# Kernel tuning notes

Measured on AMD Instinct MI355X. Metric: run time of the kernel, lower is better.

Reference implementation:

```python
import jax, jax.numpy as jnp
import numpy as np

B, L, DIM = 16, 1024, 768
HEADS, DIM_HEAD = 12, 64
INNER = HEADS * DIM_HEAD  # 768


def _make_perm(key, l, dim):
    # first `dim` entries identity, rest a random permutation of [dim, l*dim)
    tail = dim + jax.random.permutation(key, (l - 1) * dim)
    return jnp.concatenate([jnp.arange(dim), tail]).astype(jnp.int32)


def setup_inputs() -> dict:
    key = jax.random.key(0)
    kx, kq, kk, kv, ko, kp1, kp2 = jax.random.split(key, 7)
    s = DIM ** -0.5
    return {
        "x": jax.random.normal(kx, (B, L, DIM), dtype=jnp.float32),
        "Wq": jax.random.normal(kq, (DIM, INNER), dtype=jnp.float32) * s,
        "Wk": jax.random.normal(kk, (DIM, INNER), dtype=jnp.float32) * s,
        "Wv": jax.random.normal(kv, (DIM, INNER), dtype=jnp.float32) * s,
        "Wo": jax.random.normal(ko, (INNER, DIM), dtype=jnp.float32) * (INNER ** -0.5),
        "bo": jnp.zeros((DIM,), dtype=jnp.float32),
        "permq": _make_perm(kp1, L, DIM),
        "permk": _make_perm(kp2, L, DIM),
    }


def reference(x, Wq, Wk, Wv, Wo, bo, permq, permk):
    b, l, d = x.shape
    scale = DIM_HEAD ** -0.5
    flat = x.reshape(b, l * d)
    xq = flat[:, permq].reshape(b, l, d)  # irregular gather across (seq*dim)
    xk = flat[:, permk].reshape(b, l, d)
    # projections + head split: b n (h d) -> b h n d
    q = (xq @ Wq).reshape(b, l, HEADS, DIM_HEAD).transpose(0, 2, 1, 3)
    k = (xk @ Wk).reshape(b, l, HEADS, DIM_HEAD).transpose(0, 2, 1, 3)
    v = (x @ Wv).reshape(b, l, HEADS, DIM_HEAD).transpose(0, 2, 1, 3)
    dots = jnp.einsum('bhnd,bhmd->bhnm', q, k) * scale
    attn = jax.nn.softmax(dots, axis=-1)
    out = jnp.einsum('bhnm,bhmd->bhnd', attn, v)
    out = out.transpose(0, 2, 1, 3).reshape(b, l, INNER)
    return out @ Wo + bo
```

## Files before the change

kernel.cpp:

```cpp
#include <hip/hip_runtime.h>

typedef unsigned short u16;
typedef __attribute__((ext_vector_type(8))) short bf16x8;
typedef __attribute__((ext_vector_type(4))) float f32x4;
typedef __attribute__((ext_vector_type(16))) float f32x16;

#define MFMA16(a, b, c) __builtin_amdgcn_mfma_f32_16x16x32_bf16(a, b, c, 0, 0, 0)
#define MFMA32(a, b, c) __builtin_amdgcn_mfma_f32_32x32x16_bf16(a, b, c, 0, 0, 0)

#if defined(__has_builtin)
# if __has_builtin(__builtin_amdgcn_cvt_pk_bf16_f32)
#  define HAS_CVT_PK 1
# else
#  define HAS_CVT_PK 0
# endif
#else
# define HAS_CVT_PK 0
#endif

__device__ __forceinline__ u16 f2b(float f) {
    union { float f; unsigned int u; } v;
    v.f = f;
    unsigned int u = v.u;
    return (u16)((u + 0x7fffu + ((u >> 16) & 1u)) >> 16);
}

__device__ __forceinline__ unsigned int f2b_pk(float a, float b) {
#if HAS_CVT_PK
    auto r = __builtin_amdgcn_cvt_pk_bf16_f32(a, b);
    unsigned int u;
    __builtin_memcpy(&u, &r, 4);
    return u;
#else
    return (unsigned int)f2b(a) | ((unsigned int)f2b(b) << 16);
#endif
}

__device__ __forceinline__ unsigned int cvtpk_asm(float a, float b) {
    unsigned int r;
    asm("v_cvt_pk_bf16_f32 %0, %1, %2" : "=v"(r) : "v"(a), "v"(b));
    return r;
}

__device__ __forceinline__ void g2l16(const u16* gsrc, u16* ldst) {
    __builtin_amdgcn_global_load_lds(
        (const __attribute__((address_space(1))) void*)gsrc,
        (__attribute__((address_space(3))) void*)ldst,
        16, 0, 0);
}

__global__ __launch_bounds__(256) void prep_weights(
    const float* __restrict__ Wq, const float* __restrict__ Wk,
    const float* __restrict__ Wv, const float* __restrict__ Wo,
    u16* __restrict__ wqt, u16* __restrict__ wkt,
    u16* __restrict__ wvt, u16* __restrict__ wot) {
    int id = blockIdx.x * 256 + threadIdx.x;
    int k = id / 768, n = id % 768;
    int t = n * 768 + k;
    wqt[t] = f2b(Wq[id] * (0.125f * 1.44269504088896340736f));
    wkt[t] = f2b(Wk[id]);
    wvt[t] = f2b(Wv[id]);
    wot[t] = f2b(Wo[id]);
}

__global__ __launch_bounds__(256) void cast_transpose(
    const float* __restrict__ x, u16* __restrict__ xb, u16* __restrict__ xT) {
    __shared__ __attribute__((aligned(16))) u16 T[16 * 1032];
    int t = threadIdx.x;
    int j0 = blockIdx.x * 1024;
#pragma unroll
    for (int b = 0; b < 16; ++b) {
        float4 v = *(const float4*)&x[(size_t)b * 786432 + j0 + 4 * t];
        uint2 o = make_uint2(f2b_pk(v.x, v.y), f2b_pk(v.z, v.w));
        *(uint2*)&T[b * 1032 + 4 * t] = o;
        *(uint2*)&xb[(size_t)b * 786432 + j0 + 4 * t] = o;
    }
    __syncthreads();
#pragma unroll
    for (int p = 0; p < 4; ++p) {
        int jl = t + 256 * p;
        union { u16 u[16]; int4 v[2]; } r;
#pragma unroll
        for (int b = 0; b < 16; ++b) r.u[b] = T[b * 1032 + jl];
        size_t base = (size_t)(j0 + jl) * 16;
        *(int4*)&xT[base] = r.v[0];
        *(int4*)&xT[base + 8] = r.v[1];
    }
}

__global__ __launch_bounds__(256) void gather_untranspose(
    const u16* __restrict__ xT, const int* __restrict__ permq,
    const int* __restrict__ permk, u16* __restrict__ dstQ,
    u16* __restrict__ dstK) {
    __shared__ u16 T[16 * 1034];
    const int* perm = blockIdx.y ? permk : permq;
    u16* dst = blockIdx.y ? dstK : dstQ;
    int t = threadIdx.x;
    int j0 = blockIdx.x * 1024;
#pragma unroll
    for (int p = 0; p < 4; ++p) {
        int jl = p * 256 + t;
        int pq = perm[j0 + jl];
        union { u16 u[16]; int4 v[2]; } r;
        const int4* s = (const int4*)&xT[(size_t)pq * 16];
        r.v[0] = s[0];
        r.v[1] = s[1];
#pragma unroll
        for (int b = 0; b < 16; ++b) T[b * 1034 + jl] = r.u[b];
    }
    __syncthreads();
#pragma unroll
    for (int b = 0; b < 16; ++b) {
        const unsigned int* s = (const unsigned int*)&T[b * 1034 + 4 * t];
        uint2 o = make_uint2(s[0], s[1]);
        *(uint2*)&dst[(size_t)b * 786432 + j0 + 4 * t] = o;
    }
}

__device__ __forceinline__ void gemm_core(
    const u16* __restrict__ A, const u16* __restrict__ Bt,
    u16* __restrict__ Cb, float* __restrict__ Cf,
    const float* __restrict__ bias, int m0, int n0, int K, int N, int mode) {
    __shared__ __attribute__((aligned(16))) u16 As[128 * 64];
    __shared__ __attribute__((aligned(16))) u16 Bs[128 * 64];
    int tid = threadIdx.x;
    int wave = tid >> 6, lane = tid & 63;
    int lo = lane & 15, quad = lane >> 4;
    int wm = (wave >> 1) * 64, wn = (wave & 1) * 64;
    f32x4 acc[4][4] = {};

    const u16* pA[4];
    const u16* pB[4];
    u16* lA[4];
    u16* lB[4];
#pragma unroll
    for (int p = 0; p < 4; ++p) {
        int c = p * 256 + wave * 64 + lane;
        int row = c >> 3;
        int scol = ((c & 7) ^ (row & 7)) * 8;
        pA[p] = A + (size_t)(m0 + row) * K + scol;
        pB[p] = Bt + (size_t)(n0 + row) * K + scol;
        lA[p] = &As[(p * 256 + wave * 64) * 8];
        lB[p] = &Bs[(p * 256 + wave * 64) * 8];
    }

    for (int k0 = 0; k0 < K; k0 += 64) {
        __syncthreads();
#pragma unroll
        for (int p = 0; p < 4; ++p) g2l16(pA[p], lA[p]);
#pragma unroll
        for (int p = 0; p < 4; ++p) g2l16(pB[p], lB[p]);
#pragma unroll
        for (int p = 0; p < 4; ++p) { pA[p] += 64; pB[p] += 64; }
        __syncthreads();
#pragma unroll
        for (int kk = 0; kk < 2; ++kk) {
            bf16x8 af[4], bf[4];
#pragma unroll
            for (int mi = 0; mi < 4; ++mi) {
                int row = wm + mi * 16 + lo;
                af[mi] = *(const bf16x8*)&As[row * 64 + (((kk << 2) | quad) ^ (lo & 7)) * 8];
            }
#pragma unroll
            for (int nj = 0; nj < 4; ++nj) {
                int row = wn + nj * 16 + lo;
                bf[nj] = *(const bf16x8*)&Bs[row * 64 + (((kk << 2) | quad) ^ (lo & 7)) * 8];
            }
#pragma unroll
            for (int mi = 0; mi < 4; ++mi)
#pragma unroll
                for (int nj = 0; nj < 4; ++nj)
                    acc[mi][nj] = MFMA16(af[mi], bf[nj], acc[mi][nj]);
        }
    }
    if (mode == 2) {
#pragma unroll
        for (int mi = 0; mi < 4; ++mi)
#pragma unroll
            for (int nj = 0; nj < 4; ++nj) {
                int col = n0 + wn + nj * 16 + lo;
                int h = col >> 6, d = col & 63;
                int row0 = m0 + wm + mi * 16 + quad * 4;
                int bq = row0 >> 10, l = row0 & 1023;
                union { u16 u[4]; uint2 v2; } o;
#pragma unroll
                for (int r = 0; r < 4; ++r) o.u[r] = f2b(acc[mi][nj][r]);
                *(uint2*)&Cb[((size_t)((bq * 12 + h) * 64 + d)) * 1024 + l] = o.v2;
            }
        return;
    }
#pragma unroll
    for (int mi = 0; mi < 4; ++mi)
#pragma unroll
        for (int nj = 0; nj < 4; ++nj) {
            int col = n0 + wn + nj * 16 + lo;
#pragma unroll
            for (int r = 0; r < 4; ++r) {
                int row = m0 + wm + mi * 16 + quad * 4 + r;
                float v = acc[mi][nj][r];
                if (mode) Cf[(size_t)row * N + col] = v + bias[col];
                else      Cb[(size_t)row * N + col] = f2b(v);
            }
        }
}

__global__ __launch_bounds__(256) void gemm_qkv(
    const u16* __restrict__ xqb, const u16* __restrict__ wqt, u16* __restrict__ Qb,
    const u16* __restrict__ xkb, const u16* __restrict__ wkt, u16* __restrict__ Kb,
    const u16* __restrict__ xb,  const u16* __restrict__ wvt, u16* __restrict__ Vt) {
    int id = blockIdx.x;
    int xcd = id & 7, slot = id >> 3;
    int gi = slot / 6, j = slot % 6;
    int group = xcd + 8 * gi;
    int my = group & 127, z = group >> 7;
    const u16* A = (z == 0) ? xqb : (z == 1) ? xkb : xb;
    const u16* W = (z == 0) ? wqt : (z == 1) ? wkt : wvt;
    u16* C = (z == 0) ? Qb : (z == 1) ? Kb : Vt;
    gemm_core(A, W, C, nullptr, nullptr, my * 128, j * 128, 768, 768,
              (z == 2) ? 2 : 0);
}

__global__ __launch_bounds__(256) void gemm_out(
    const u16* __restrict__ A, const u16* __restrict__ Bt,
    float* __restrict__ Cf, const float* __restrict__ bias) {
    int id = blockIdx.x;
    int xcd = id & 7, slot = id >> 3;
    int gi = slot / 6, j = slot % 6;
    int group = xcd + 8 * gi;
    gemm_core(A, Bt, nullptr, Cf, bias, group * 128, j * 128, 768, 768, 1);
}

#define LDK 72
__global__ __launch_bounds__(256) void flash_attn(
    const u16* __restrict__ Qb, const u16* __restrict__ Kb,
    const u16* __restrict__ Vt, u16* __restrict__ AO) {
    __shared__ __attribute__((aligned(16))) u16 Ks[64 * LDK];
    __shared__ __attribute__((aligned(16))) u16 Vs[64 * LDK];
    int id = blockIdx.x;
    int bh = (id & 7) + ((id >> 6) << 3);
    int qt = (id >> 3) & 7;
    int b = bh / 12, h = bh % 12;
    int tid = threadIdx.x, wave = tid >> 6, lane = tid & 63;
    int ln = lane & 31, hi = lane >> 5;
    int q0 = qt * 128;

    bf16x8 qa[4];
    {
        const u16* qrow = &Qb[(size_t)(b * 1024 + q0 + wave * 32 + ln) * 768 + h * 64 + hi * 8];
#pragma unroll
        for (int kk = 0; kk < 4; ++kk)
            qa[kk] = *(const bf16x8*)&qrow[kk * 16];
    }

    const float M2 = 24.0f;
    float l_own = 0.0f;
    f32x16 acc_o[2] = {};
    const size_t kbase = (size_t)b * 1024 * 768 + h * 64;
    const size_t vbase = (size_t)bh * 64 * 1024;
    int srow = tid >> 3, sco = (tid & 7) * 8;

    int4 kr0 = *(const int4*)&Kb[kbase + (size_t)srow * 768 + sco];
    int4 kr1 = *(const int4*)&Kb[kbase + (size_t)(srow + 32) * 768 + sco];
    int4 vr0 = *(const int4*)&Vt[vbase + (size_t)srow * 1024 + sco];
    int4 vr1 = *(const int4*)&Vt[vbase + (size_t)(srow + 32) * 1024 + sco];

    for (int t = 0; t < 16; ++t) {
        __syncthreads();
        *(int4*)&Ks[srow * LDK + sco] = kr0;
        *(int4*)&Ks[(srow + 32) * LDK + sco] = kr1;
        *(int4*)&Vs[srow * LDK + sco] = vr0;
        *(int4*)&Vs[(srow + 32) * LDK + sco] = vr1;
        __syncthreads();
        int tn = (t + 1) & 15;
        kr0 = *(const int4*)&Kb[kbase + (size_t)(tn * 64 + srow) * 768 + sco];
        kr1 = *(const int4*)&Kb[kbase + (size_t)(tn * 64 + srow + 32) * 768 + sco];
        vr0 = *(const int4*)&Vt[vbase + (size_t)srow * 1024 + tn * 64 + sco];
        vr1 = *(const int4*)&Vt[vbase + (size_t)(srow + 32) * 1024 + tn * 64 + sco];
        f32x16 sacc[2] = {};
#pragma unroll
        for (int nj = 0; nj < 2; ++nj)
#pragma unroll
            for (int kk = 0; kk < 4; ++kk) {
                bf16x8 kb = *(const bf16x8*)&Ks[(ln + 32 * nj) * LDK + kk * 16 + hi * 8];
                sacc[nj] = MFMA32(kb, qa[kk], sacc[nj]);
            }
#pragma unroll
        for (int nj = 0; nj < 2; ++nj) {
            float p[16];
#pragma unroll
            for (int r = 0; r < 16; ++r)
                p[r] = __builtin_amdgcn_exp2f(sacc[nj][r] - M2);
            l_own += (((p[0] + p[1]) + (p[2] + p[3])) + ((p[4] + p[5]) + (p[6] + p[7])))
                   + (((p[8] + p[9]) + (p[10] + p[11])) + ((p[12] + p[13]) + (p[14] + p[15])));
            unsigned int c[8];
#pragma unroll
            for (int m = 0; m < 8; ++m)
                c[m] = cvtpk_asm(p[2 * m], p[2 * m + 1]);
            asm("v_permlane32_swap_b32 %0, %1" : "+v"(c[0]), "+v"(c[2]));
            asm("v_permlane32_swap_b32 %0, %1" : "+v"(c[1]), "+v"(c[3]));
            asm("v_permlane32_swap_b32 %0, %1" : "+v"(c[4]), "+v"(c[6]));
            asm("v_permlane32_swap_b32 %0, %1" : "+v"(c[5]), "+v"(c[7]));
            union { unsigned int w[4]; bf16x8 v; } pa0, pa1;
            pa0.w[0] = c[0]; pa0.w[1] = c[1]; pa0.w[2] = c[2]; pa0.w[3] = c[3];
            pa1.w[0] = c[4]; pa1.w[1] = c[5]; pa1.w[2] = c[6]; pa1.w[3] = c[7];
#pragma unroll
            for (int njd = 0; njd < 2; ++njd) {
                bf16x8 vb0 = *(const bf16x8*)&Vs[(ln + 32 * njd) * LDK + (2 * nj) * 16 + hi * 8];
                acc_o[njd] = MFMA32(pa0.v, vb0, acc_o[njd]);
            }
#pragma unroll
            for (int njd = 0; njd < 2; ++njd) {
                bf16x8 vb1 = *(const bf16x8*)&Vs[(ln + 32 * njd) * LDK + (2 * nj + 1) * 16 + hi * 8];
                acc_o[njd] = MFMA32(pa1.v, vb1, acc_o[njd]);
            }
        }
    }
    float l = l_own + __shfl_xor(l_own, 32, 64);
    float inv = 1.0f / l;
#pragma unroll
    for (int r = 0; r < 16; ++r) {
        int qrow = (r & 3) + 8 * (r >> 2) + 4 * hi;
        float invq = __shfl(inv, qrow, 64);
        int row = b * 1024 + q0 + wave * 32 + qrow;
#pragma unroll
        for (int njd = 0; njd < 2; ++njd)
            AO[(size_t)row * 768 + h * 64 + ln + 32 * njd] = f2b(acc_o[njd][r] * invq);
    }
}

static const size_t SZ_W  = (size_t)768 * 768 * 2;
static const size_t SZ_X  = (size_t)16 * 1024 * 768 * 2;
static const size_t OFF_WQT = 0;
static const size_t OFF_WKT = SZ_W;
static const size_t OFF_WVT = 2 * SZ_W;
static const size_t OFF_WOT = 3 * SZ_W;
static const size_t OFF_XB  = 4 * SZ_W;
static const size_t OFF_XQB = OFF_XB  + SZ_X;
static const size_t OFF_XKB = OFF_XQB + SZ_X;
static const size_t OFF_QB  = OFF_XKB + SZ_X;
static const size_t OFF_KB  = OFF_QB  + SZ_X;
static const size_t OFF_VT  = OFF_KB  + SZ_X;
static const size_t OFF_XT  = OFF_QB;
static const size_t OFF_AO  = OFF_XKB;

extern "C" void kernel_launch(void* const* d_in, const int* in_sizes, int n_in,
                              void* d_out, int out_size, void* d_ws, size_t ws_size,
                              hipStream_t stream) {
    const float* x  = (const float*)d_in[0];
    const float* Wq = (const float*)d_in[1];
    const float* Wk = (const float*)d_in[2];
    const float* Wv = (const float*)d_in[3];
    const float* Wo = (const float*)d_in[4];
    const float* bo = (const float*)d_in[5];
    const int* permq = (const int*)d_in[6];
    const int* permk = (const int*)d_in[7];
    float* out = (float*)d_out;
    char* ws = (char*)d_ws;
    u16* wqt = (u16*)(ws + OFF_WQT);
    u16* wkt = (u16*)(ws + OFF_WKT);
    u16* wvt = (u16*)(ws + OFF_WVT);
    u16* wot = (u16*)(ws + OFF_WOT);
    u16* xb  = (u16*)(ws + OFF_XB);
    u16* xqb = (u16*)(ws + OFF_XQB);
    u16* xkb = (u16*)(ws + OFF_XKB);
    u16* Qb  = (u16*)(ws + OFF_QB);
    u16* Kb  = (u16*)(ws + OFF_KB);
    u16* Vt  = (u16*)(ws + OFF_VT);
    u16* xT  = (u16*)(ws + OFF_XT);
    u16* AO  = (u16*)(ws + OFF_AO);

    prep_weights<<<2304, 256, 0, stream>>>(Wq, Wk, Wv, Wo, wqt, wkt, wvt, wot);
    cast_transpose<<<768, 256, 0, stream>>>(x, xb, xT);
    gather_untranspose<<<dim3(768, 2), 256, 0, stream>>>(xT, permq, permk, xqb, xkb);
    gemm_qkv<<<2304, 256, 0, stream>>>(xqb, wqt, Qb, xkb, wkt, Kb, xb, wvt, Vt);
    flash_attn<<<1536, 256, 0, stream>>>(Qb, Kb, Vt, AO);
    gemm_out<<<768, 256, 0, stream>>>(AO, wot, out, bo);
}
```

Baseline: 351.9 us.

## Widen attention blocks to 256 queries and split V projection into own launch

The flash attention kernel now runs 512 threads (8 waves) per block covering 256 query rows, so each K/V tile staged in shared memory is reused by twice as many queries. Each thread loads one row of K and V per tile instead of two, and the block-to-(batch,head) mapping is rearranged for XCD locality. The fused QKV projection is split into a separate V GEMM and a Q/K GEMM, with the V GEMM launched before the Q/K one. The larger blocks halve the grid and may lower occupancy, and the extra launch adds some overhead.

```diff
diff --git a/kernel.cpp b/kernel.cpp
--- a/kernel.cpp
+++ b/kernel.cpp
@@ -204,20 +204,27 @@
         }
 }
 
-__global__ __launch_bounds__(256) void gemm_qkv(
+__global__ __launch_bounds__(256) void gemm_qk(
     const u16* __restrict__ xqb, const u16* __restrict__ wqt, u16* __restrict__ Qb,
-    const u16* __restrict__ xkb, const u16* __restrict__ wkt, u16* __restrict__ Kb,
-    const u16* __restrict__ xb,  const u16* __restrict__ wvt, u16* __restrict__ Vt) {
+    const u16* __restrict__ xkb, const u16* __restrict__ wkt, u16* __restrict__ Kb) {
     int id = blockIdx.x;
     int xcd = id & 7, slot = id >> 3;
     int gi = slot / 6, j = slot % 6;
     int group = xcd + 8 * gi;
     int my = group & 127, z = group >> 7;
-    const u16* A = (z == 0) ? xqb : (z == 1) ? xkb : xb;
-    const u16* W = (z == 0) ? wqt : (z == 1) ? wkt : wvt;
-    u16* C = (z == 0) ? Qb : (z == 1) ? Kb : Vt;
-    gemm_core(A, W, C, nullptr, nullptr, my * 128, j * 128, 768, 768,
-              (z == 2) ? 2 : 0);
+    const u16* A = z ? xkb : xqb;
+    const u16* W = z ? wkt : wqt;
+    u16* C = z ? Kb : Qb;
+    gemm_core(A, W, C, nullptr, nullptr, my * 128, j * 128, 768, 768, 0);
+}
+
+__global__ __launch_bounds__(256) void gemm_v(
+    const u16* __restrict__ xb, const u16* __restrict__ wvt, u16* __restrict__ Vt) {
+    int id = blockIdx.x;
+    int xcd = id & 7, slot = id >> 3;
+    int gi = slot / 6, j = slot % 6;
+    int group = xcd + 8 * gi;
+    gemm_core(xb, wvt, Vt, nullptr, nullptr, group * 128, j * 128, 768, 768, 2);
 }
 
 __global__ __launch_bounds__(256) void gemm_out(
@@ -231,18 +238,19 @@
 }
 
 #define LDK 72
-__global__ __launch_bounds__(256) void flash_attn(
+__global__ __launch_bounds__(512) void flash_attn(
     const u16* __restrict__ Qb, const u16* __restrict__ Kb,
     const u16* __restrict__ Vt, u16* __restrict__ AO) {
     __shared__ __attribute__((aligned(16))) u16 Ks[64 * LDK];
     __shared__ __attribute__((aligned(16))) u16 Vs[64 * LDK];
     int id = blockIdx.x;
-    int bh = (id & 7) + ((id >> 6) << 3);
-    int qt = (id >> 3) & 7;
+    int xcd = id & 7, slot = id >> 3;
+    int bh = xcd + 8 * (slot % 24);
+    int qt = slot / 24;
     int b = bh / 12, h = bh % 12;
     int tid = threadIdx.x, wave = tid >> 6, lane = tid & 63;
     int ln = lane & 31, hi = lane >> 5;
-    int q0 = qt * 128;
+    int q0 = qt * 256;
 
     bf16x8 qa[4];
     {
@@ -259,23 +267,17 @@
     const size_t vbase = (size_t)bh * 64 * 1024;
     int srow = tid >> 3, sco = (tid & 7) * 8;
 
-    int4 kr0 = *(const int4*)&Kb[kbase + (size_t)srow * 768 + sco];
-    int4 kr1 = *(const int4*)&Kb[kbase + (size_t)(srow + 32) * 768 + sco];
-    int4 vr0 = *(const int4*)&Vt[vbase + (size_t)srow * 1024 + sco];
-    int4 vr1 = *(const int4*)&Vt[vbase + (size_t)(srow + 32) * 1024 + sco];
+    int4 kr = *(const int4*)&Kb[kbase + (size_t)srow * 768 + sco];
+    int4 vr = *(const int4*)&Vt[vbase + (size_t)srow * 1024 + sco];
 
     for (int t = 0; t < 16; ++t) {
         __syncthreads();
-        *(int4*)&Ks[srow * LDK + sco] = kr0;
-        *(int4*)&Ks[(srow + 32) * LDK + sco] = kr1;
-        *(int4*)&Vs[srow * LDK + sco] = vr0;
-        *(int4*)&Vs[(srow + 32) * LDK + sco] = vr1;
+        *(int4*)&Ks[srow * LDK + sco] = kr;
+        *(int4*)&Vs[srow * LDK + sco] = vr;
         __syncthreads();
         int tn = (t + 1) & 15;
-        kr0 = *(const int4*)&Kb[kbase + (size_t)(tn * 64 + srow) * 768 + sco];
-        kr1 = *(const int4*)&Kb[kbase + (size_t)(tn * 64 + srow + 32) * 768 + sco];
-        vr0 = *(const int4*)&Vt[vbase + (size_t)srow * 1024 + tn * 64 + sco];
-        vr1 = *(const int4*)&Vt[vbase + (size_t)(srow + 32) * 1024 + tn * 64 + sco];
+        kr = *(const int4*)&Kb[kbase + (size_t)(tn * 64 + srow) * 768 + sco];
+        vr = *(const int4*)&Vt[vbase + (size_t)srow * 1024 + tn * 64 + sco];
         f32x16 sacc[2] = {};
 #pragma unroll
         for (int nj = 0; nj < 2; ++nj)
@@ -372,7 +374,8 @@
     prep_weights<<<2304, 256, 0, stream>>>(Wq, Wk, Wv, Wo, wqt, wkt, wvt, wot);
     cast_transpose<<<768, 256, 0, stream>>>(x, xb, xT);
     gather_untranspose<<<dim3(768, 2), 256, 0, stream>>>(xT, permq, permk, xqb, xkb);
-    gemm_qkv<<<2304, 256, 0, stream>>>(xqb, wqt, Qb, xkb, wkt, Kb, xb, wvt, Vt);
-    flash_attn<<<1536, 256, 0, stream>>>(Qb, Kb, Vt, AO);
+    gemm_v<<<768, 256, 0, stream>>>(xb, wvt, Vt);
+    gemm_qk<<<1536, 256, 0, stream>>>(xqb, wqt, Qb, xkb, wkt, Kb);
+    flash_attn<<<768, 512, 0, stream>>>(Qb, Kb, Vt, AO);
     gemm_out<<<768, 256, 0, stream>>>(AO, wot, out, bo);
 }
```

Measured after the change: 354.0 us. Within noise of the previous version (+0.6%).
